# Kernel tuning notes

Hardware: AMD Instinct MI355X
Metric: run time of the kernel (lower is better)

## Reference

```python
import jax, jax.numpy as jnp
import numpy as np

EMB_DIM, D_H, BSZ, SEQ = 2048, 128, 4, 4096
HALF = D_H // 2


def apply_rope(x, sin, cos):
    # x: [b, s, d]; sin/cos: [s, d//2]; interleaved-pair rotation
    b, s, d = x.shape
    xr = x.reshape(b, s, d // 2, 2)
    x0, x1 = xr[..., 0], xr[..., 1]
    r0 = x0 * cos - x1 * sin
    r1 = x1 * cos + x0 * sin
    return jnp.stack([r0, r1], axis=-1).reshape(b, s, d)


def setup_inputs() -> dict:
    key = jax.random.key(0)
    kx, kq, kk, kv = jax.random.split(key, 4)
    x = jax.random.normal(kx, (BSZ, SEQ, EMB_DIM), dtype=jnp.float32)
    # causal mask (1 = attend, 0 = masked), matching mask[q,:] slicing in source
    mask = jnp.tril(jnp.ones((SEQ, SEQ), dtype=jnp.int32))
    # standard RoPE angle tables: [seq, d_h//2]
    inv_freq = 1.0 / (10000.0 ** (jnp.arange(HALF, dtype=jnp.float32) / HALF))
    angles = jnp.arange(SEQ, dtype=jnp.float32)[:, None] * inv_freq[None, :]
    sin, cos = jnp.sin(angles), jnp.cos(angles)
    scale = 1.0 / np.sqrt(EMB_DIM)
    W_Q = jax.random.normal(kq, (EMB_DIM, D_H), dtype=jnp.float32) * scale
    W_K = jax.random.normal(kk, (EMB_DIM, D_H), dtype=jnp.float32) * scale
    W_V = jax.random.normal(kv, (EMB_DIM, D_H), dtype=jnp.float32) * scale
    return {"x": x, "mask": mask, "sin": sin, "cos": cos,
            "W_Q": W_Q, "W_K": W_K, "W_V": W_V}


def reference(x, mask, sin, cos, W_Q, W_V, W_K):
    # QKV projections
    Q = apply_rope(x @ W_Q, sin, cos)  # [b, s, d_h]
    K = apply_rope(x @ W_K, sin, cos)  # [b, s, d_h]
    V = x @ W_V                        # [b, s, d_h]
    # The source's chunked loop is exactly full masked attention over all K/V.
    scores = jnp.einsum('bqd,bkd->bqk', Q, K) / jnp.sqrt(jnp.float32(D_H))
    scores = jnp.where(mask[None, :, :] == 0, -jnp.inf, scores)
    attn = jax.nn.softmax(scores, axis=-1)
    return jnp.einsum('bqk,bkd->bqd', attn, V)
```

## Files before the change

### kernel.cpp

```cpp
#include <hip/hip_runtime.h>
#include <stdint.h>
#include <stddef.h>

typedef __bf16 bf16;
typedef __bf16 bf16x8 __attribute__((ext_vector_type(8)));
typedef float f32x4 __attribute__((ext_vector_type(4)));
typedef unsigned int uint32x2 __attribute__((ext_vector_type(2)));
typedef unsigned int uint32x4 __attribute__((ext_vector_type(4)));

typedef const __attribute__((address_space(1))) uint32_t GU32;
typedef __attribute__((address_space(3))) uint32_t LU32;

__device__ __forceinline__ f32x4 mfma16(bf16x8 a, bf16x8 b, f32x4 c) {
  return __builtin_amdgcn_mfma_f32_16x16x32_bf16(a, b, c, 0, 0, 0);
}
__device__ __forceinline__ void gload16(const void* g, void* l) {
  __builtin_amdgcn_global_load_lds((GU32*)g, (LU32*)l, 16, 0, 0);
}

__global__ __launch_bounds__(256) void k_prep(const float* __restrict__ Wq,
                                              const float* __restrict__ Wk,
                                              const float* __restrict__ Wv,
                                              bf16* __restrict__ Wct) {
  __shared__ float tile[64][65];
  const int tid = threadIdx.x;
  const int widx = blockIdx.x >> 6, rem = blockIdx.x & 63;
  const int k0 = (rem >> 1) * 64, n0 = (rem & 1) * 64;
  const float* W = (widx == 0) ? Wq : (widx == 1) ? Wk : Wv;
  const int rg = tid >> 4, cq = tid & 15;
#pragma unroll
  for (int i = 0; i < 4; ++i) {
    int krow = i * 16 + rg;
    f32x4 v = *(const f32x4*)(W + (size_t)(k0 + krow) * 128 + n0 + cq * 4);
#pragma unroll
    for (int j = 0; j < 4; ++j) tile[krow][cq * 4 + j] = v[j];
  }
  __syncthreads();
#pragma unroll
  for (int i = 0; i < 4; ++i) {
    int nrow = i * 16 + rg;
    union { bf16 h[4]; uint32x2 u; } pk;
#pragma unroll
    for (int j = 0; j < 4; ++j) pk.h[j] = (bf16)tile[cq * 4 + j][nrow];
    *(uint32x2*)(Wct + (size_t)(widx * 128 + n0 + nrow) * 2048 + k0 + cq * 4) = pk.u;
  }
}

__global__ __launch_bounds__(512, 1) void k_proj(
    const float* __restrict__ x, const float* __restrict__ sint, const float* __restrict__ cost,
    const bf16* __restrict__ Wct, bf16* __restrict__ Qg, bf16* __restrict__ Kg,
    bf16* __restrict__ Vtg) {
  __shared__ __align__(16) uint8_t smem[114688];
  const int tid = threadIdx.x;
  const int lane = tid & 63, w = tid >> 6;
  const int l15 = lane & 15, l16 = lane >> 4;
  const int mb = blockIdx.x;
  const int arow = tid >> 3, aj = tid & 7;

  f32x4 acc[4][3] = {};
  f32x4 regA[2], regB[2];

  const float* abase = x + (size_t)(mb * 64 + arow) * 2048 + aj * 8;

  auto stageB = [&](int buf, int ks) {
    uint8_t* bbm = smem + 16384 + buf * 49152;
    int k0 = ks * 64;
#pragma unroll
    for (int i = 0; i < 6; ++i) {
      int L = i * 8192 + tid * 16;
      int n = L >> 7, cp = (L >> 4) & 7;
      int cc = cp ^ (n & 7);
      const uint8_t* src = (const uint8_t*)Wct + (((size_t)n * 2048 + k0 + cc * 8) << 1);
      gload16(src, bbm + i * 8192 + w * 1024);
    }
  };
  auto loadA = [&](int ks, f32x4* r) {
    const f32x4* p = (const f32x4*)(abase + ks * 64);
    r[0] = p[0];
    r[1] = p[1];
  };
  auto writeA = [&](int buf, const f32x4* r) {
    uint8_t* ab = smem + buf * 8192;
    union { bf16 v[8]; uint32x4 u; } pk;
#pragma unroll
    for (int e = 0; e < 8; ++e) pk.v[e] = (bf16)r[e >> 2][e & 3];
    *(uint32x4*)(ab + arow * 128 + (((aj ^ (arow & 7)) & 7) << 4)) = pk.u;
  };
  auto compute = [&](int buf) {
    uint8_t* ab = smem + buf * 8192;
    uint8_t* bbm = smem + 16384 + buf * 49152;
    bf16x8 af[2][4], bv[2][3];
#pragma unroll
    for (int kk = 0; kk < 2; ++kk) {
#pragma unroll
      for (int mt = 0; mt < 4; ++mt) {
        int ml = mt * 16 + l15;
        af[kk][mt] = *(const bf16x8*)(ab + ml * 128 + (((kk * 4 + l16) ^ (ml & 7)) << 4));
      }
#pragma unroll
      for (int nt = 0; nt < 3; ++nt) {
        int nl = w * 48 + nt * 16 + l15;
        bv[kk][nt] = *(const bf16x8*)(bbm + nl * 128 + (((kk * 4 + l16) ^ (nl & 7)) << 4));
      }
    }
    __builtin_amdgcn_s_setprio(1);
#pragma unroll
    for (int kk = 0; kk < 2; ++kk)
#pragma unroll
      for (int mt = 0; mt < 4; ++mt)
#pragma unroll
        for (int nt = 0; nt < 3; ++nt)
          acc[mt][nt] = mfma16(af[kk][mt], bv[kk][nt], acc[mt][nt]);
    __builtin_amdgcn_s_setprio(0);
  };

  loadA(0, regA);
  stageB(0, 0);
  loadA(1, regB);
  writeA(0, regA);
  asm volatile("s_waitcnt vmcnt(2)" ::: "memory");
  asm volatile("s_waitcnt lgkmcnt(0)" ::: "memory");
  __builtin_amdgcn_s_barrier();

  for (int ks = 0; ks < 30; ks += 2) {
    {
      stageB(1, ks + 1);
      loadA(ks + 2, regA);
      compute(0);
      writeA(1, regB);
      asm volatile("s_waitcnt vmcnt(2)" ::: "memory");
      asm volatile("s_waitcnt lgkmcnt(0)" ::: "memory");
      __builtin_amdgcn_s_barrier();
    }
    {
      stageB(0, ks + 2);
      loadA(ks + 3, regB);
      compute(1);
      writeA(0, regA);
      asm volatile("s_waitcnt vmcnt(2)" ::: "memory");
      asm volatile("s_waitcnt lgkmcnt(0)" ::: "memory");
      __builtin_amdgcn_s_barrier();
    }
  }
  {
    stageB(1, 31);
    compute(0);
    writeA(1, regB);
    asm volatile("s_waitcnt vmcnt(0)" ::: "memory");
    asm volatile("s_waitcnt lgkmcnt(0)" ::: "memory");
    __builtin_amdgcn_s_barrier();
  }
  compute(1);

  const int bb = mb >> 6;
#pragma unroll
  for (int mt = 0; mt < 4; ++mt) {
    int gm = mb * 64 + mt * 16 + l16 * 4;
    int s0 = gm & 4095;
#pragma unroll
    for (int nt = 0; nt < 3; ++nt) {
      int jcol = w * 48 + nt * 16 + l15;
      f32x4 v = acc[mt][nt];
      if (jcol < 256) {
        int p = (jcol & 127) >> 1;
        bool even = ((jcol & 1) == 0);
#pragma unroll
        for (int r = 0; r < 4; ++r) {
          float pv = __shfl_xor(v[r], 1);
          int s = s0 + r;
          float cs = cost[s * 64 + p], sn = sint[s * 64 + p];
          float nv = even ? (v[r] * cs - pv * sn) : (v[r] * cs + pv * sn);
          bf16 hb = (bf16)nv;
          if (jcol < 128) Qg[((size_t)(bb << 12) + s) * 128 + jcol] = hb;
          else            Kg[((size_t)(bb << 12) + s) * 128 + jcol - 128] = hb;
        }
      } else {
        int d = jcol - 256;
        union { bf16 h[4]; uint32x2 u; } pk;
#pragma unroll
        for (int r = 0; r < 4; ++r) pk.h[r] = (bf16)v[r];
        *(uint32x2*)((uint8_t*)Vtg + (((size_t)(bb << 7) + d) * 4096 + s0) * 2) = pk.u;
      }
    }
  }
}

__global__ __launch_bounds__(256, 2) void k_attn(
    const bf16* __restrict__ Qg, const bf16* __restrict__ Kg, const bf16* __restrict__ Vtg,
    float* __restrict__ PO, float* __restrict__ ML) {
  __shared__ __align__(16) uint8_t smem[81920];
  const int tid = threadIdx.x;
  const int lane = tid & 63, w = tid >> 6;
  const int l15 = lane & 15, l16 = lane >> 4;

  int gid = blockIdx.x;
  int b = gid / 80, rr = gid % 80;
  int j, c;
  if (rr < 8)       { j = rr;                 c = 0; }
  else if (rr < 24) { j = 8 + ((rr - 8) >> 1);  c = (rr - 8) & 1; }
  else if (rr < 48) { j = 16 + (rr - 24) / 3;   c = (rr - 24) % 3; }
  else              { j = 24 + ((rr - 48) >> 2); c = (rr - 48) & 3; }

  const int q0w = j * 128 + w * 32;
  const int kv_lo = c * 1024;
  const int kv_hi = min((c + 1) * 1024, (j + 1) * 128);
  const int T = (kv_hi - kv_lo) >> 6;

  bf16x8 qf[2][4];
#pragma unroll
  for (int qt = 0; qt < 2; ++qt)
#pragma unroll
    for (int kk = 0; kk < 4; ++kk)
      qf[qt][kk] = *(const bf16x8*)(Qg + ((size_t)(b << 12) + q0w + qt * 16 + l15) * 128 + kk * 32 + l16 * 8);

  f32x4 o[2][8] = {};
  float m_r[2] = {-1e30f, -1e30f};
  float l_r[2] = {0.f, 0.f};
  uint8_t* pb = smem + 65536 + w * 4096;

  auto stage = [&](int t) {
    uint8_t* kb = smem + (t & 1) * 32768;
    uint8_t* vb = kb + 16384;
    int kv0 = kv_lo + t * 64;
#pragma unroll
    for (int i = 0; i < 4; ++i) {
      int L = i * 4096 + tid * 16;
      {
        int kv = L >> 8, cp = (L >> 4) & 15, cc = cp ^ (kv & 7);
        const uint8_t* src = (const uint8_t*)Kg + ((size_t)((b << 12) + kv0 + kv) << 8) + (cc << 4);
        gload16(src, kb + i * 4096 + w * 1024);
      }
      {
        int d = L >> 7, cp = (L >> 4) & 7, cc = cp ^ (d & 7);
        const uint8_t* src = (const uint8_t*)Vtg + ((size_t)(((b << 7) + d) << 12) + kv0 + (cc << 3)) * 2;
        gload16(src, vb + i * 4096 + w * 1024);
      }
    }
  };

  stage(0);
  __syncthreads();

  for (int t = 0; t < T; ++t) {
    if (t + 1 < T) stage(t + 1);
    const int kv0 = kv_lo + t * 64;
    if (kv0 <= q0w + 31) {
      uint8_t* kb = smem + (t & 1) * 32768;
      uint8_t* vb = kb + 16384;
      f32x4 sfr[4][2] = {};
#pragma unroll
      for (int kk = 0; kk < 4; ++kk) {
#pragma unroll
        for (int kvt = 0; kvt < 4; ++kvt) {
          int kvl = kvt * 16 + l15;
          bf16x8 kf = *(const bf16x8*)(kb + (kvl << 8) + (((kk * 4 + l16) ^ (kvl & 7)) << 4));
#pragma unroll
          for (int qt = 0; qt < 2; ++qt)
            sfr[kvt][qt] = mfma16(kf, qf[qt][kk], sfr[kvt][qt]);
        }
      }
      const bool need_mask = (kv0 + 63 > q0w);
      const float scale = 0.08838834764831845f;
#pragma unroll
      for (int qt = 0; qt < 2; ++qt) {
        const int q = q0w + qt * 16 + l15;
        float pvv[4][4];
        float tmax = -1e30f;
#pragma unroll
        for (int kvt = 0; kvt < 4; ++kvt)
#pragma unroll
          for (int r = 0; r < 4; ++r) {
            float sv = sfr[kvt][qt][r] * scale;
            if (need_mask) {
              int kv = kv0 + kvt * 16 + l16 * 4 + r;
              if (kv > q) sv = -1e30f;
            }
            pvv[kvt][r] = sv;
            tmax = fmaxf(tmax, sv);
          }
        tmax = fmaxf(tmax, __shfl_xor(tmax, 16));
        tmax = fmaxf(tmax, __shfl_xor(tmax, 32));
        float mnew = fmaxf(m_r[qt], tmax);
        float corr = __expf(m_r[qt] - mnew);
        m_r[qt] = mnew;
        float rs = 0.f;
#pragma unroll
        for (int kvt = 0; kvt < 4; ++kvt)
#pragma unroll
          for (int r = 0; r < 4; ++r) {
            float p = __expf(pvv[kvt][r] - mnew);
            pvv[kvt][r] = p;
            rs += p;
          }
        rs += __shfl_xor(rs, 16);
        rs += __shfl_xor(rs, 32);
        l_r[qt] = l_r[qt] * corr + rs;
        const int qrow = qt * 16 + l15;
#pragma unroll
        for (int kvt = 0; kvt < 4; ++kvt) {
          union { bf16 h[4]; uint32x2 u; } pk;
#pragma unroll
          for (int r = 0; r < 4; ++r) pk.h[r] = (bf16)pvv[kvt][r];
          int kv2 = kvt * 32 + l16 * 8;
          *(uint32x2*)(pb + qrow * 128 + ((((kv2 >> 4) ^ (qrow & 7)) << 4) | (kv2 & 15))) = pk.u;
        }
#pragma unroll
        for (int r = 0; r < 4; ++r) {
          float cr = __shfl(corr, l16 * 4 + r);
#pragma unroll
          for (int dt = 0; dt < 8; ++dt) o[qt][dt][r] *= cr;
        }
      }
#pragma unroll
      for (int kvb = 0; kvb < 2; ++kvb) {
        bf16x8 pa[2];
#pragma unroll
        for (int qt = 0; qt < 2; ++qt) {
          int qrow = qt * 16 + l15;
          int kv2 = kvb * 64 + l16 * 16;
          pa[qt] = *(const bf16x8*)(pb + qrow * 128 + (((kv2 >> 4) ^ (qrow & 7)) << 4));
        }
#pragma unroll
        for (int dt = 0; dt < 8; ++dt) {
          int d = dt * 16 + l15;
          bf16x8 vf = *(const bf16x8*)(vb + (d << 7) + (((kvb * 4 + l16) ^ (d & 7)) << 4));
#pragma unroll
          for (int qt = 0; qt < 2; ++qt)
            o[qt][dt] = mfma16(pa[qt], vf, o[qt][dt]);
        }
      }
    }
    __syncthreads();
  }

  float* POb = PO + (size_t)((b * 32 + j) * 4 + c) * 16384;
#pragma unroll
  for (int qt = 0; qt < 2; ++qt)
#pragma unroll
    for (int dt = 0; dt < 8; ++dt)
#pragma unroll
      for (int r = 0; r < 4; ++r)
        POb[(w * 32 + qt * 16 + l16 * 4 + r) * 128 + dt * 16 + l15] = o[qt][dt][r];
  float* MLb = ML + (size_t)((b * 32 + j) * 4 + c) * 256;
  if (l16 == 0) {
#pragma unroll
    for (int qt = 0; qt < 2; ++qt) {
      MLb[w * 32 + qt * 16 + l15] = m_r[qt];
      MLb[128 + w * 32 + qt * 16 + l15] = l_r[qt];
    }
  }
}

__global__ void k_combine(const float* __restrict__ PO, const float* __restrict__ ML,
                          float* __restrict__ out) {
  int blk = blockIdx.x;
  int b = blk >> 5, j = blk & 31;
  int nc = 1 + (j >> 3);
  int t = threadIdx.x;
  int q = t >> 1, half = t & 1;
  const float* MLb = ML + (size_t)(b * 32 + j) * 4 * 256;
  float mv[4], lv[4];
  float ms = -1e30f;
  for (int cc = 0; cc < nc; ++cc) {
    mv[cc] = MLb[cc * 256 + q];
    lv[cc] = MLb[cc * 256 + 128 + q];
    ms = fmaxf(ms, mv[cc]);
  }
  float wgt[4];
  float den = 0.f;
  for (int cc = 0; cc < nc; ++cc) { wgt[cc] = __expf(mv[cc] - ms); den += wgt[cc] * lv[cc]; }
  float inv = 1.f / den;
  const float* POb = PO + (size_t)(b * 32 + j) * 4 * 16384 + q * 128 + half * 64;
  float* ob = out + ((size_t)(b << 12) + j * 128 + q) * 128 + half * 64;
  for (int d = 0; d < 64; d += 4) {
    f32x4 a = {0.f, 0.f, 0.f, 0.f};
    for (int cc = 0; cc < nc; ++cc) {
      f32x4 v = *(const f32x4*)(POb + cc * 16384 + d);
      a += v * wgt[cc];
    }
    a *= inv;
    *(f32x4*)(ob + d) = a;
  }
}

extern "C" void kernel_launch(void* const* d_in, const int* in_sizes, int n_in,
                              void* d_out, int out_size, void* d_ws, size_t ws_size,
                              hipStream_t stream) {
  const float* x = (const float*)d_in[0];
  const float* sint = (const float*)d_in[2];
  const float* cost = (const float*)d_in[3];
  const float* Wq = (const float*)d_in[4];
  const float* Wk = (const float*)d_in[5];
  const float* Wv = (const float*)d_in[6];
  uint8_t* ws = (uint8_t*)d_ws;

  bf16* Wct = (bf16*)(ws + 0x0);
  bf16* Qg  = (bf16*)(ws + 0x180000);
  bf16* Kg  = (bf16*)(ws + 0x580000);
  bf16* Vtg = (bf16*)(ws + 0x980000);
  float* PO = (float*)(ws + 0xD80000);
  float* ML = (float*)(ws + 0x2D80000);
  float* out = (float*)d_out;

  hipLaunchKernelGGL(k_prep, dim3(192), dim3(256), 0, stream, Wq, Wk, Wv, Wct);
  hipLaunchKernelGGL(k_proj, dim3(256), dim3(512), 0, stream, x, sint, cost, Wct, Qg, Kg, Vtg);
  hipLaunchKernelGGL(k_attn, dim3(320), dim3(256), 0, stream, Qg, Kg, Vtg, PO, ML);
  hipLaunchKernelGGL(k_combine, dim3(128), dim3(256), 0, stream, PO, ML, out);
}
```

Baseline: 130.1 us.

## Pre-swizzle weights into MFMA fragment order and pad A tile in LDS

The prep kernel now writes the bf16 weights in the exact per-lane MFMA fragment order for each 64-wide k-step, so the projection kernel stages B with contiguous 16-byte global-to-LDS copies and reads fragments as lane*16 offsets with no XOR swizzle math. The A tile in LDS moves from an XOR-swizzled layout to a padded fragment-major layout (stride 17), and the LDS footprint grows slightly. This targets address computation and bank conflicts in the projection GEMM, and it couples the weight layout tightly to the MFMA tile shape.

```diff
diff --git a/kernel.cpp b/kernel.cpp
--- a/kernel.cpp
+++ b/kernel.cpp
@@ -21,7 +21,7 @@
 __global__ __launch_bounds__(256) void k_prep(const float* __restrict__ Wq,
                                               const float* __restrict__ Wk,
                                               const float* __restrict__ Wv,
-                                              bf16* __restrict__ Wct) {
+                                              bf16* __restrict__ WA) {
   __shared__ float tile[64][65];
   const int tid = threadIdx.x;
   const int widx = blockIdx.x >> 6, rem = blockIdx.x & 63;
@@ -37,20 +37,27 @@
   }
   __syncthreads();
 #pragma unroll
-  for (int i = 0; i < 4; ++i) {
-    int nrow = i * 16 + rg;
-    union { bf16 h[4]; uint32x2 u; } pk;
-#pragma unroll
-    for (int j = 0; j < 4; ++j) pk.h[j] = (bf16)tile[cq * 4 + j][nrow];
-    *(uint32x2*)(Wct + (size_t)(widx * 128 + n0 + nrow) * 2048 + k0 + cq * 4) = pk.u;
+  for (int gi = 0; gi < 2; ++gi) {
+    int G = tid * 2 + gi;
+    int n_local = G >> 3, kg = G & 7;
+    union { bf16 h[8]; uint32x4 u; } pk;
+#pragma unroll
+    for (int j = 0; j < 8; ++j) pk.h[j] = (bf16)tile[kg * 8 + j][n_local];
+    int n_glob = widx * 128 + n0 + n_local;
+    int k_glob = k0 + kg * 8;
+    int ks = k_glob >> 6, kl = k_glob & 63;
+    int kk = kl >> 5, l16g = (kl >> 3) & 3;
+    int ng = n_glob >> 4, l15g = n_glob & 15;
+    size_t gaddr = (size_t)ks * 3072 + (size_t)((ng * 2 + kk) * 64 + l16g * 16 + l15g);
+    *(uint32x4*)((uint8_t*)WA + gaddr * 16) = pk.u;
   }
 }
 
 __global__ __launch_bounds__(512, 1) void k_proj(
     const float* __restrict__ x, const float* __restrict__ sint, const float* __restrict__ cost,
-    const bf16* __restrict__ Wct, bf16* __restrict__ Qg, bf16* __restrict__ Kg,
+    const bf16* __restrict__ WA, bf16* __restrict__ Qg, bf16* __restrict__ Kg,
     bf16* __restrict__ Vtg) {
-  __shared__ __align__(16) uint8_t smem[114688];
+  __shared__ __align__(16) uint8_t smem[115712];
   const int tid = threadIdx.x;
   const int lane = tid & 63, w = tid >> 6;
   const int l15 = lane & 15, l16 = lane >> 4;
@@ -61,18 +68,15 @@
   f32x4 regA[2], regB[2];
 
   const float* abase = x + (size_t)(mb * 64 + arow) * 2048 + aj * 8;
+  const uint8_t* wbase = (const uint8_t*)WA;
+  const int agw = ((arow >> 4) * 2 + (aj >> 2)) * 68 + (aj & 3) * 17 + (arow & 15);
 
   auto stageB = [&](int buf, int ks) {
-    uint8_t* bbm = smem + 16384 + buf * 49152;
-    int k0 = ks * 64;
-#pragma unroll
-    for (int i = 0; i < 6; ++i) {
-      int L = i * 8192 + tid * 16;
-      int n = L >> 7, cp = (L >> 4) & 7;
-      int cc = cp ^ (n & 7);
-      const uint8_t* src = (const uint8_t*)Wct + (((size_t)n * 2048 + k0 + cc * 8) << 1);
-      gload16(src, bbm + i * 8192 + w * 1024);
-    }
+    uint8_t* bbm = smem + 17408 + buf * 49152;
+    const uint8_t* src = wbase + (size_t)ks * 49152 + tid * 16;
+#pragma unroll
+    for (int i = 0; i < 6; ++i)
+      gload16(src + i * 8192, bbm + i * 8192 + tid * 16);
   };
   auto loadA = [&](int ks, f32x4* r) {
     const f32x4* p = (const f32x4*)(abase + ks * 64);
@@ -80,28 +84,24 @@
     r[1] = p[1];
   };
   auto writeA = [&](int buf, const f32x4* r) {
-    uint8_t* ab = smem + buf * 8192;
+    uint8_t* ab = smem + buf * 8704;
     union { bf16 v[8]; uint32x4 u; } pk;
 #pragma unroll
     for (int e = 0; e < 8; ++e) pk.v[e] = (bf16)r[e >> 2][e & 3];
-    *(uint32x4*)(ab + arow * 128 + (((aj ^ (arow & 7)) & 7) << 4)) = pk.u;
+    *(uint32x4*)(ab + (agw << 4)) = pk.u;
   };
   auto compute = [&](int buf) {
-    uint8_t* ab = smem + buf * 8192;
-    uint8_t* bbm = smem + 16384 + buf * 49152;
+    uint8_t* ab = smem + buf * 8704;
+    uint8_t* bbm = smem + 17408 + buf * 49152;
     bf16x8 af[2][4], bv[2][3];
 #pragma unroll
     for (int kk = 0; kk < 2; ++kk) {
 #pragma unroll
-      for (int mt = 0; mt < 4; ++mt) {
-        int ml = mt * 16 + l15;
-        af[kk][mt] = *(const bf16x8*)(ab + ml * 128 + (((kk * 4 + l16) ^ (ml & 7)) << 4));
-      }
-#pragma unroll
-      for (int nt = 0; nt < 3; ++nt) {
-        int nl = w * 48 + nt * 16 + l15;
-        bv[kk][nt] = *(const bf16x8*)(bbm + nl * 128 + (((kk * 4 + l16) ^ (nl & 7)) << 4));
-      }
+      for (int mt = 0; mt < 4; ++mt)
+        af[kk][mt] = *(const bf16x8*)(ab + (((mt * 2 + kk) * 68 + l16 * 17 + l15) << 4));
+#pragma unroll
+      for (int nt = 0; nt < 3; ++nt)
+        bv[kk][nt] = *(const bf16x8*)(bbm + ((((w * 3 + nt) * 2 + kk) << 10) + lane * 16));
     }
     __builtin_amdgcn_s_setprio(1);
 #pragma unroll
@@ -394,7 +394,7 @@
   const float* Wv = (const float*)d_in[6];
   uint8_t* ws = (uint8_t*)d_ws;
 
-  bf16* Wct = (bf16*)(ws + 0x0);
+  bf16* WA  = (bf16*)(ws + 0x0);
   bf16* Qg  = (bf16*)(ws + 0x180000);
   bf16* Kg  = (bf16*)(ws + 0x580000);
   bf16* Vtg = (bf16*)(ws + 0x980000);
@@ -402,8 +402,8 @@
   float* ML = (float*)(ws + 0x2D80000);
   float* out = (float*)d_out;
 
-  hipLaunchKernelGGL(k_prep, dim3(192), dim3(256), 0, stream, Wq, Wk, Wv, Wct);
-  hipLaunchKernelGGL(k_proj, dim3(256), dim3(512), 0, stream, x, sint, cost, Wct, Qg, Kg, Vtg);
+  hipLaunchKernelGGL(k_prep, dim3(192), dim3(256), 0, stream, Wq, Wk, Wv, WA);
+  hipLaunchKernelGGL(k_proj, dim3(256), dim3(512), 0, stream, x, sint, cost, WA, Qg, Kg, Vtg);
   hipLaunchKernelGGL(k_attn, dim3(320), dim3(256), 0, stream, Qg, Kg, Vtg, PO, ML);
   hipLaunchKernelGGL(k_combine, dim3(128), dim3(256), 0, stream, PO, ML, out);
 }
```

After: 130.4 us. About the same (+0.3%).
